# Kernel tuning notes

Measured on AMD Instinct MI355X. Metric: run time of the kernel, lower is better.

## Reference

```python
import jax, jax.numpy as jnp
import numpy as np

N = 50000
E = 800000
IN_C = 128
HID = 8
OUT_C = 32
HEADS = (4, 4, 4)
NEG_SLOPE = 0.2


def gat_conv(x, src, dst, W, att_src, att_dst, bias, heads, out_c, concat):
    # x: [N, F_in]; W: [F_in, heads*out_c]; att_*: [heads, out_c]; bias: [heads*out_c] or [out_c]
    n = x.shape[0]
    h = (x @ W).reshape(n, heads, out_c)                      # [N, H, C]
    a_src = (h * att_src).sum(-1)                             # [N, H]
    a_dst = (h * att_dst).sum(-1)                             # [N, H]
    e = jax.nn.leaky_relu(a_src[src] + a_dst[dst], NEG_SLOPE)  # [E, H]
    # segment softmax over edges grouped by destination node
    m = jax.ops.segment_max(e, dst, num_segments=n)           # [N, H]
    m = jnp.where(jnp.isfinite(m), m, 0.0)
    p = jnp.exp(e - m[dst])                                   # [E, H]
    s = jax.ops.segment_sum(p, dst, num_segments=n)           # [N, H]
    alpha = p / (s[dst] + 1e-16)                              # [E, H]
    msg = h[src] * alpha[:, :, None]                          # [E, H, C]
    out = jax.ops.segment_sum(msg, dst, num_segments=n)       # [N, H, C]
    out = out.reshape(n, heads * out_c) if concat else out.mean(axis=1)
    return out + bias


def setup_inputs() -> dict:
    key = jax.random.key(0)
    ks = jax.random.split(key, 16)
    x = jax.random.normal(ks[0], (N, IN_C), dtype=jnp.float32)
    edge_index = jax.random.randint(ks[1], (2, E), 0, N, dtype=jnp.int64)
    c1 = HID                       # per-head out of conv1 (8)
    c2 = HID * HEADS[0]            # per-head out of conv2 (32)
    c3 = OUT_C                     # per-head out of conv3 (32)
    in2 = HID * HEADS[0]           # 32
    in3 = HID * HEADS[0] * HEADS[1]  # 128
    sc = 0.1
    return {
        "x": x,
        "edge_index": edge_index,
        "W1": jax.random.normal(ks[2], (IN_C, HEADS[0] * c1), dtype=jnp.float32) * sc,
        "as1": jax.random.normal(ks[3], (HEADS[0], c1), dtype=jnp.float32) * sc,
        "ad1": jax.random.normal(ks[4], (HEADS[0], c1), dtype=jnp.float32) * sc,
        "b1": jnp.zeros((HEADS[0] * c1,), dtype=jnp.float32),
        "W2": jax.random.normal(ks[5], (in2, HEADS[1] * c2), dtype=jnp.float32) * sc,
        "as2": jax.random.normal(ks[6], (HEADS[1], c2), dtype=jnp.float32) * sc,
        "ad2": jax.random.normal(ks[7], (HEADS[1], c2), dtype=jnp.float32) * sc,
        "b2": jnp.zeros((HEADS[1] * c2,), dtype=jnp.float32),
        "W3": jax.random.normal(ks[8], (in3, HEADS[2] * c3), dtype=jnp.float32) * sc,
        "as3": jax.random.normal(ks[9], (HEADS[2], c3), dtype=jnp.float32) * sc,
        "ad3": jax.random.normal(ks[10], (HEADS[2], c3), dtype=jnp.float32) * sc,
        "b3": jnp.zeros((c3,), dtype=jnp.float32),
    }


def reference(x, edge_index, W1, as1, ad1, b1, W2, as2, ad2, b2, W3, as3, ad3, b3):
    src, dst = edge_index[0], edge_index[1]
    h = gat_conv(x, src, dst, W1, as1, ad1, b1, HEADS[0], HID, True)
    h = jax.nn.elu(h)
    h = gat_conv(h, src, dst, W2, as2, ad2, b2, HEADS[1], HID * HEADS[0], True)
    h = jax.nn.elu(h)
    out = gat_conv(h, src, dst, W3, as3, ad3, b3, HEADS[2], OUT_C, False)
    return out
```

## Files before the change

kernel.cpp:

```cpp
#include <hip/hip_runtime.h>
#include <hip/hip_fp16.h>

#define NEG_SLOPE 0.2f

static inline int cdiv(long long a, long long b) { return (int)((a + b - 1) / b); }

typedef _Float16 f16x8 __attribute__((ext_vector_type(8)));
typedef float f32x4 __attribute__((ext_vector_type(4)));

__device__ __forceinline__ float4 f4_add(float4 a, float4 b) {
    return make_float4(a.x + b.x, a.y + b.y, a.z + b.z, a.w + b.w);
}
__device__ __forceinline__ float4 f4_leaky(float4 a) {
    return make_float4(a.x > 0.f ? a.x : NEG_SLOPE * a.x,
                       a.y > 0.f ? a.y : NEG_SLOPE * a.y,
                       a.z > 0.f ? a.z : NEG_SLOPE * a.z,
                       a.w > 0.f ? a.w : NEG_SLOPE * a.w);
}
__device__ __forceinline__ float4 f4_exp(float4 e) {
    return make_float4(__expf(e.x), __expf(e.y), __expf(e.z), __expf(e.w));
}
__device__ __forceinline__ float f4_get(float4 v, int i) {
    return i == 0 ? v.x : i == 1 ? v.y : i == 2 ? v.z : v.w;
}

union h4u {
    float2  f2;
    __half2 h2[2];
};

__device__ __forceinline__ void load_sd(const void* ei_raw, int is64, int e, int E_,
                                        int& s, int& d)
{
    if (is64) {
        const long long* p = (const long long*)ei_raw;
        s = (int)p[e];
        d = (int)p[E_ + e];
    } else {
        const int* p = (const int*)ei_raw;
        s = p[e];
        d = p[E_ + e];
    }
}

__global__ __launch_bounds__(256) void prep_kernel(
    const void* __restrict__ ei, int E_, int n, int* __restrict__ flag,
    int* __restrict__ deg,
    const float* __restrict__ W1, __half* __restrict__ Wt1,
    const float* __restrict__ W2, __half* __restrict__ Wt2,
    const float* __restrict__ W3, __half* __restrict__ Wt3)
{
    int idx = blockIdx.x * 256 + threadIdx.x;

    if (blockIdx.x == 0) {
        __shared__ int bad;
        if (threadIdx.x == 0) bad = 0;
        __syncthreads();
        const long long* e64 = (const long long*)ei;
        int cnt = E_ < 512 ? E_ : 512;
        bool ok = true;
        for (int i = threadIdx.x; i < cnt; i += 256) {
            long long v = e64[i];
            if (v < 0 || v >= n) ok = false;
        }
        if (!ok) atomicAdd(&bad, 1);
        __syncthreads();
        if (threadIdx.x == 0) *flag = (bad == 0) ? 1 : 0;
    }

    if (idx < n) deg[idx] = 0;

    if (idx < 128 * 32) {
        int k = idx / 32, c = idx % 32;
        Wt1[c * 128 + k] = __float2half(W1[idx]);
    }
    if (idx < 32 * 128) {
        int k = idx / 128, c = idx % 128;
        Wt2[c * 32 + k] = __float2half(W2[idx]);
    }
    if (idx < 128 * 128) {
        int k = idx / 128, c = idx % 128;
        Wt3[c * 128 + k] = __float2half(W3[idx]);
    }
}

__global__ __launch_bounds__(256) void hist_kernel(const void* __restrict__ ei_raw,
                                                   const int* __restrict__ flag,
                                                   int* __restrict__ deg,
                                                   int* __restrict__ s32,
                                                   int* __restrict__ d32,
                                                   int* __restrict__ rank, int E_)
{
    int base = blockIdx.x * 1024 + threadIdx.x;
    int is64 = *flag;
    int sj[4], dj[4], rj[4];
    bool v[4];
#pragma unroll
    for (int j = 0; j < 4; j++) {
        int e = base + j * 256;
        v[j] = e < E_;
        if (v[j]) load_sd(ei_raw, is64, e, E_, sj[j], dj[j]);
    }
#pragma unroll
    for (int j = 0; j < 4; j++) {
        int e = base + j * 256;
        if (v[j]) { s32[e] = sj[j]; d32[e] = dj[j]; }
    }
#pragma unroll
    for (int j = 0; j < 4; j++) {
        if (v[j]) rj[j] = atomicAdd(deg + dj[j], 1);
    }
#pragma unroll
    for (int j = 0; j < 4; j++) {
        int e = base + j * 256;
        if (v[j]) rank[e] = rj[j];
    }
}

__device__ __forceinline__ int wave_incl_scan(int v)
{
    int lane = threadIdx.x & 63;
#pragma unroll
    for (int off = 1; off < 64; off <<= 1) {
        int t = __shfl_up(v, off);
        if (lane >= off) v += t;
    }
    return v;
}

__global__ __launch_bounds__(1024) void scan_part_kernel(const int* __restrict__ deg,
                                                         int* __restrict__ start,
                                                         int* __restrict__ bsum, int n)
{
    __shared__ int wsum[16];
    int i = blockIdx.x * 1024 + threadIdx.x;
    int wid = threadIdx.x >> 6, lane = threadIdx.x & 63;
    int v = (i < n) ? deg[i] : 0;
    int incl = wave_incl_scan(v);
    if (lane == 63) wsum[wid] = incl;
    __syncthreads();
    if (wid == 0) {
        int w = (lane < 16) ? wsum[lane] : 0;
        w = wave_incl_scan(w);
        if (lane < 16) wsum[lane] = w;
    }
    __syncthreads();
    int excl = incl - v + (wid ? wsum[wid - 1] : 0);
    if (i < n) start[i] = excl;
    if (threadIdx.x == 1023) bsum[blockIdx.x] = wsum[15];
}

__global__ __launch_bounds__(1024) void scan_add_kernel(const int* __restrict__ deg,
                                                        const int* __restrict__ bsum,
                                                        int* __restrict__ start, int n)
{
    __shared__ int off_sh;
    if (threadIdx.x == 0) {
        int s = 0;
        for (int j = 0; j < blockIdx.x; j++) s += bsum[j];
        off_sh = s;
    }
    __syncthreads();
    int i = blockIdx.x * 1024 + threadIdx.x;
    if (i >= n) return;
    int v = start[i] + off_sh;
    start[i] = v;
    if (i == n - 1) start[n] = v + deg[i];
}

__global__ __launch_bounds__(256) void scatter_kernel(const int* __restrict__ s32,
                                                      const int* __restrict__ d32,
                                                      const int* __restrict__ rank,
                                                      const int* __restrict__ start,
                                                      int* __restrict__ sorted_src, int E_)
{
    int base = blockIdx.x * 1024 + threadIdx.x;
    int sj[4], dj[4], rj[4];
    bool v[4];
#pragma unroll
    for (int j = 0; j < 4; j++) {
        int e = base + j * 256;
        v[j] = e < E_;
        sj[j] = v[j] ? s32[e] : 0;
        dj[j] = v[j] ? d32[e] : 0;
        rj[j] = v[j] ? rank[e] : 0;
    }
    int pj[4];
#pragma unroll
    for (int j = 0; j < 4; j++) {
        if (v[j]) pj[j] = start[dj[j]] + rj[j];
    }
#pragma unroll
    for (int j = 0; j < 4; j++) {
        if (v[j]) __builtin_nontemporal_store(sj[j], sorted_src + pj[j]);
    }
}

template <int K, int NOUT, int A16>
__global__ __launch_bounds__(256) void gemm_mfma_kernel(
    const void* __restrict__ xin, const __half* __restrict__ Wt,
    const float* __restrict__ att_s, const float* __restrict__ att_d,
    __half* __restrict__ h, float* __restrict__ a_s, float* __restrict__ a_d, int n)
{
    constexpr int KC = 32;
    constexpr int NT = NOUT / 16;
    constexpr int XP = KC + 8;
    constexpr int HP = NOUT + 8;
    constexpr int C  = NOUT / 4;

    __shared__ _Float16 Xs[64 * XP];
    __shared__ _Float16 Ws[NOUT * XP];
    __shared__ _Float16 Hs[64 * HP];
    __shared__ float As[NOUT], Ad[NOUT];

    const int tid  = threadIdx.x;
    const int nb   = blockIdx.x * 64;
    const int wave = tid >> 6, lane = tid & 63;
    const int m16  = lane & 15, quad = lane >> 4;

    if (tid < NOUT) { As[tid] = att_s[tid]; Ad[tid] = att_d[tid]; }

    f32x4 acc[NT];
#pragma unroll
    for (int t = 0; t < NT; t++) acc[t] = (f32x4){0.f, 0.f, 0.f, 0.f};

    for (int kc = 0; kc < K; kc += KC) {
        {
            int node = tid >> 2, seg = tid & 3;
            int gn = nb + node;
            f16x8 v = {0, 0, 0, 0, 0, 0, 0, 0};
            if (gn < n) {
                if (A16) {
                    v = *(const f16x8*)((const __half*)xin + (size_t)gn * K + kc +
                                        seg * 8);
                } else {
                    const float4* p =
                        (const float4*)((const float*)xin + (size_t)gn * K + kc + seg * 8);
                    float4 a = p[0], b = p[1];
                    v = (f16x8){(_Float16)a.x, (_Float16)a.y, (_Float16)a.z,
                                (_Float16)a.w, (_Float16)b.x, (_Float16)b.y,
                                (_Float16)b.z, (_Float16)b.w};
                }
            }
            *(f16x8*)&Xs[node * XP + seg * 8] = v;
        }
        for (int u = tid; u < NOUT * 4; u += 256) {
            int col = u >> 2, seg = u & 3;
            *(f16x8*)&Ws[col * XP + seg * 8] =
                *(const f16x8*)(Wt + (size_t)col * K + kc + seg * 8);
        }
        __syncthreads();

        f16x8 a = *(const f16x8*)&Xs[(wave * 16 + m16) * XP + quad * 8];
#pragma unroll
        for (int t = 0; t < NT; t++) {
            f16x8 b = *(const f16x8*)&Ws[(t * 16 + m16) * XP + quad * 8];
            acc[t] = __builtin_amdgcn_mfma_f32_16x16x32_f16(a, b, acc[t], 0, 0, 0);
        }
        __syncthreads();
    }

#pragma unroll
    for (int t = 0; t < NT; t++) {
#pragma unroll
        for (int r = 0; r < 4; r++) {
            int row = wave * 16 + quad * 4 + r;
            Hs[row * HP + t * 16 + m16] = (_Float16)acc[t][r];
        }
    }
    __syncthreads();

    for (int u = tid; u < 64 * NOUT / 8; u += 256) {
        int row = u / (NOUT / 8), seg = u % (NOUT / 8);
        int gn = nb + row;
        if (gn < n)
            *(f16x8*)(h + (size_t)gn * NOUT + seg * 8) =
                *(const f16x8*)&Hs[row * HP + seg * 8];
    }

    {
        int node = tid >> 2, head = tid & 3;
        int gn = nb + node;
        const _Float16* hr = &Hs[node * HP + head * C];
        float s1 = 0.f, s2 = 0.f;
#pragma unroll 4
        for (int c = 0; c < C; c++) {
            float v = (float)hr[c];
            s1 += v * As[head * C + c];
            s2 += v * Ad[head * C + c];
        }
        if (gn < n) {
            a_s[gn * 4 + head] = s1;
            a_d[gn * 4 + head] = s2;
        }
    }
}

template <int MODE>
__global__ __launch_bounds__(256) void gat_agg128_kernel(
    const int* __restrict__ start, const int* __restrict__ sorted_src,
    const __half* __restrict__ h, const float* __restrict__ a_s,
    const float* __restrict__ a_d, const float* __restrict__ bias,
    void* __restrict__ out, int n)
{
    constexpr int MAXD = 64;
    __shared__ float  p_sh[8][MAXD * 4];
    __shared__ float4 invs_sh[8];

    int local = threadIdx.x >> 5;
    int q     = threadIdx.x & 31;
    int node  = blockIdx.x * 8 + local;
    bool active = node < n;
    int s0 = 0, s1 = 0;
    if (active) { s0 = start[node]; s1 = start[node + 1]; }
    int deg = s1 - s0;

    const float4* as4 = (const float4*)a_s;
    float4 ad = active ? ((const float4*)a_d)[node] : make_float4(0.f, 0.f, 0.f, 0.f);

    float4 sm = make_float4(0.f, 0.f, 0.f, 0.f);
    for (int i = s0 + q; i < s1; i += 32) {
        int s = sorted_src[i];
        float4 p = f4_exp(f4_leaky(f4_add(as4[s], ad)));
        sm = f4_add(sm, p);
        int j = i - s0;
        if (j < MAXD) ((float4*)&p_sh[local][0])[j] = p;
    }
#pragma unroll
    for (int off = 16; off; off >>= 1) {
        sm.x += __shfl_xor(sm.x, off, 32);
        sm.y += __shfl_xor(sm.y, off, 32);
        sm.z += __shfl_xor(sm.z, off, 32);
        sm.w += __shfl_xor(sm.w, off, 32);
    }
    if (q == 0) {
        invs_sh[local] = make_float4(1.f / (sm.x + 1e-16f), 1.f / (sm.y + 1e-16f),
                                     1.f / (sm.z + 1e-16f), 1.f / (sm.w + 1e-16f));
    }
    __syncthreads();

    int head = q >> 3;
    float invh = f4_get(invs_sh[local], head);
    const float2* __restrict__ h2 = (const float2*)h + q;
    const float* __restrict__ pl = &p_sh[local][0];

    float4 acc = make_float4(0.f, 0.f, 0.f, 0.f);
    if (deg <= MAXD) {
        int i = 0;
        for (; i + 8 <= deg; i += 8) {
            int   sj[8];
            float aj[8];
#pragma unroll
            for (int j = 0; j < 8; j++) sj[j] = sorted_src[s0 + i + j];
#pragma unroll
            for (int j = 0; j < 8; j++) aj[j] = pl[(i + j) * 4 + head] * invh;
            float2 rj[8];
#pragma unroll
            for (int j = 0; j < 8; j++) rj[j] = h2[(size_t)sj[j] * 32];
#pragma unroll
            for (int j = 0; j < 8; j++) {
                h4u u; u.f2 = rj[j];
                float2 lo = __half22float2(u.h2[0]);
                float2 hi = __half22float2(u.h2[1]);
                acc.x += lo.x * aj[j]; acc.y += lo.y * aj[j];
                acc.z += hi.x * aj[j]; acc.w += hi.y * aj[j];
            }
        }
        for (; i < deg; i++) {
            h4u u; u.f2 = h2[(size_t)sorted_src[s0 + i] * 32];
            float a = pl[i * 4 + head] * invh;
            float2 lo = __half22float2(u.h2[0]);
            float2 hi = __half22float2(u.h2[1]);
            acc.x += lo.x * a; acc.y += lo.y * a; acc.z += hi.x * a; acc.w += hi.y * a;
        }
    } else {
        for (int i = s0; i < s1; i++) {
            int s = sorted_src[i];
            float4 p = f4_exp(f4_leaky(f4_add(as4[s], ad)));
            float a = f4_get(p, head) * invh;
            h4u u; u.f2 = h2[(size_t)s * 32];
            float2 lo = __half22float2(u.h2[0]);
            float2 hi = __half22float2(u.h2[1]);
            acc.x += lo.x * a; acc.y += lo.y * a; acc.z += hi.x * a; acc.w += hi.y * a;
        }
    }

    if (MODE == 0) {
        if (active) {
            float4 b4 = ((const float4*)bias)[q];
            float4 v = f4_add(acc, b4);
            v.x = v.x > 0.f ? v.x : (__expf(v.x) - 1.f);
            v.y = v.y > 0.f ? v.y : (__expf(v.y) - 1.f);
            v.z = v.z > 0.f ? v.z : (__expf(v.z) - 1.f);
            v.w = v.w > 0.f ? v.w : (__expf(v.w) - 1.f);
            h4u u;
            u.h2[0] = __floats2half2_rn(v.x, v.y);
            u.h2[1] = __floats2half2_rn(v.z, v.w);
            *(float2*)((__half*)out + (size_t)node * 128 + q * 4) = u.f2;
        }
    } else {
        __shared__ float4 sh4[8][33];
        sh4[local][q] = acc;
        __syncthreads();
        if (q < 8 && active) {
            float4 a = sh4[local][q];
            float4 b = sh4[local][q + 8];
            float4 c = sh4[local][q + 16];
            float4 d = sh4[local][q + 24];
            float4 b4 = ((const float4*)bias)[q];
            float4 r = make_float4(0.25f * (a.x + b.x + c.x + d.x) + b4.x,
                                   0.25f * (a.y + b.y + c.y + d.y) + b4.y,
                                   0.25f * (a.z + b.z + c.z + d.z) + b4.z,
                                   0.25f * (a.w + b.w + c.w + d.w) + b4.w);
            *(float4*)((float*)out + (size_t)node * 32 + q * 4) = r;
        }
    }
}

__global__ __launch_bounds__(256) void gat_agg32_kernel(
    const int* __restrict__ start, const int* __restrict__ sorted_src,
    const __half* __restrict__ h, const float* __restrict__ a_s,
    const float* __restrict__ a_d, const float* __restrict__ bias,
    __half* __restrict__ out, int n)
{
    constexpr int MAXD = 32;
    __shared__ float  p_sh[32][MAXD * 4];
    __shared__ float4 invs_sh[32];

    int local = threadIdx.x >> 3;
    int q     = threadIdx.x & 7;
    int node  = blockIdx.x * 32 + local;
    bool active = node < n;
    int s0 = 0, s1 = 0;
    if (active) { s0 = start[node]; s1 = start[node + 1]; }
    int deg = s1 - s0;

    const float4* as4 = (const float4*)a_s;
    float4 ad = active ? ((const float4*)a_d)[node] : make_float4(0.f, 0.f, 0.f, 0.f);

    float4 sm = make_float4(0.f, 0.f, 0.f, 0.f);
    for (int i = s0 + q; i < s1; i += 8) {
        int s = sorted_src[i];
        float4 p = f4_exp(f4_leaky(f4_add(as4[s], ad)));
        sm = f4_add(sm, p);
        int j = i - s0;
        if (j < MAXD) ((float4*)&p_sh[local][0])[j] = p;
    }
#pragma unroll
    for (int off = 4; off; off >>= 1) {
        sm.x += __shfl_xor(sm.x, off, 8);
        sm.y += __shfl_xor(sm.y, off, 8);
        sm.z += __shfl_xor(sm.z, off, 8);
        sm.w += __shfl_xor(sm.w, off, 8);
    }
    if (q == 0) {
        invs_sh[local] = make_float4(1.f / (sm.x + 1e-16f), 1.f / (sm.y + 1e-16f),
                                     1.f / (sm.z + 1e-16f), 1.f / (sm.w + 1e-16f));
    }
    __syncthreads();

    int head = q >> 1;
    float invh = f4_get(invs_sh[local], head);
    const float2* __restrict__ h2 = (const float2*)h + q;
    const float* __restrict__ pl = &p_sh[local][0];

    float4 acc = make_float4(0.f, 0.f, 0.f, 0.f);
    if (deg <= MAXD) {
        int i = 0;
        for (; i + 8 <= deg; i += 8) {
            int   sj[8];
            float aj[8];
#pragma unroll
            for (int j = 0; j < 8; j++) sj[j] = sorted_src[s0 + i + j];
#pragma unroll
            for (int j = 0; j < 8; j++) aj[j] = pl[(i + j) * 4 + head] * invh;
            float2 rj[8];
#pragma unroll
            for (int j = 0; j < 8; j++) rj[j] = h2[(size_t)sj[j] * 8];
#pragma unroll
            for (int j = 0; j < 8; j++) {
                h4u u; u.f2 = rj[j];
                float2 lo = __half22float2(u.h2[0]);
                float2 hi = __half22float2(u.h2[1]);
                acc.x += lo.x * aj[j]; acc.y += lo.y * aj[j];
                acc.z += hi.x * aj[j]; acc.w += hi.y * aj[j];
            }
        }
        for (; i < deg; i++) {
            h4u u; u.f2 = h2[(size_t)sorted_src[s0 + i] * 8];
            float a = pl[i * 4 + head] * invh;
            float2 lo = __half22float2(u.h2[0]);
            float2 hi = __half22float2(u.h2[1]);
            acc.x += lo.x * a; acc.y += lo.y * a; acc.z += hi.x * a; acc.w += hi.y * a;
        }
    } else {
        for (int i = s0; i < s1; i++) {
            int s = sorted_src[i];
            float4 p = f4_exp(f4_leaky(f4_add(as4[s], ad)));
            float a = f4_get(p, head) * invh;
            h4u u; u.f2 = h2[(size_t)s * 8];
            float2 lo = __half22float2(u.h2[0]);
            float2 hi = __half22float2(u.h2[1]);
            acc.x += lo.x * a; acc.y += lo.y * a; acc.z += hi.x * a; acc.w += hi.y * a;
        }
    }

    if (active) {
        float4 b4 = ((const float4*)bias)[q];
        float4 v = f4_add(acc, b4);
        v.x = v.x > 0.f ? v.x : (__expf(v.x) - 1.f);
        v.y = v.y > 0.f ? v.y : (__expf(v.y) - 1.f);
        v.z = v.z > 0.f ? v.z : (__expf(v.z) - 1.f);
        v.w = v.w > 0.f ? v.w : (__expf(v.w) - 1.f);
        h4u u;
        u.h2[0] = __floats2half2_rn(v.x, v.y);
        u.h2[1] = __floats2half2_rn(v.z, v.w);
        *(float2*)(out + (size_t)node * 32 + q * 4) = u.f2;
    }
}


extern "C" void kernel_launch(void* const* d_in, const int* in_sizes, int n_in,
                              void* d_out, int out_size, void* d_ws, size_t ws_size,
                              hipStream_t stream)
{
    const float* x   = (const float*)d_in[0];
    const void*  ei  = d_in[1];
    const float* W1  = (const float*)d_in[2];
    const float* as1 = (const float*)d_in[3];
    const float* ad1 = (const float*)d_in[4];
    const float* b1  = (const float*)d_in[5];
    const float* W2  = (const float*)d_in[6];
    const float* as2 = (const float*)d_in[7];
    const float* ad2 = (const float*)d_in[8];
    const float* b2  = (const float*)d_in[9];
    const float* W3  = (const float*)d_in[10];
    const float* as3 = (const float*)d_in[11];
    const float* ad3 = (const float*)d_in[12];
    const float* b3  = (const float*)d_in[13];
    float* out = (float*)d_out;

    const int N_ = in_sizes[0] / 128;
    const int E_ = in_sizes[1] / 2;

    char* ws = (char*)d_ws;
    size_t off = 0;
    auto alloc = [&](size_t nbytes) -> void* {
        void* p = ws + off;
        off += (nbytes + 255) & ~(size_t)255;
        return p;
    };
    __half* h         = (__half*)alloc((size_t)N_ * 128 * 2);
    __half* x2h       = (__half*)alloc((size_t)N_ * 32 * 2);
    __half* x3h       = (__half*)alloc((size_t)N_ * 128 * 2);
    __half* Wt1       = (__half*)alloc(128 * 32 * 2);
    __half* Wt2       = (__half*)alloc(32 * 128 * 2);
    __half* Wt3       = (__half*)alloc(128 * 128 * 2);
    float* asrc       = (float*)alloc((size_t)N_ * 4 * 4);
    float* adst       = (float*)alloc((size_t)N_ * 4 * 4);
    int*   deg        = (int*)alloc((size_t)N_ * 4);
    int*   start      = (int*)alloc((size_t)(N_ + 1) * 4);
    int*   sorted_src = (int*)alloc((size_t)E_ * 4);
    int*   s32        = (int*)alloc((size_t)E_ * 4);
    int*   d32        = (int*)alloc((size_t)E_ * 4);
    int*   rank       = (int*)alloc((size_t)E_ * 4);
    int*   bsum       = (int*)alloc(4096);
    int*   flag       = (int*)alloc(256);

    const int gN8  = cdiv(N_, 8);
    const int gN32 = cdiv(N_, 32);
    const int gN64 = cdiv(N_, 64);
    const int nSB  = cdiv(N_, 1024);
    int prepWork = N_ > 128 * 128 ? N_ : 128 * 128;

    prep_kernel<<<cdiv(prepWork, 256), 256, 0, stream>>>(ei, E_, N_, flag, deg,
                                                         W1, Wt1, W2, Wt2, W3, Wt3);
    hist_kernel<<<cdiv(E_, 1024), 256, 0, stream>>>(ei, flag, deg, s32, d32, rank, E_);
    scan_part_kernel<<<nSB, 1024, 0, stream>>>(deg, start, bsum, N_);
    scan_add_kernel<<<nSB, 1024, 0, stream>>>(deg, bsum, start, N_);
    scatter_kernel<<<cdiv(E_, 1024), 256, 0, stream>>>(s32, d32, rank, start,
                                                       sorted_src, E_);

    gemm_mfma_kernel<128, 32, 0><<<gN64, 256, 0, stream>>>(x, Wt1, as1, ad1, h,
                                                           asrc, adst, N_);
    gat_agg32_kernel<<<gN32, 256, 0, stream>>>(start, sorted_src, h, asrc, adst, b1,
                                               x2h, N_);

    gemm_mfma_kernel<32, 128, 1><<<gN64, 256, 0, stream>>>(x2h, Wt2, as2, ad2, h,
                                                           asrc, adst, N_);
    gat_agg128_kernel<0><<<gN8, 256, 0, stream>>>(start, sorted_src, h, asrc, adst, b2,
                                                  x3h, N_);

    gemm_mfma_kernel<128, 128, 1><<<gN64, 256, 0, stream>>>(x3h, Wt3, as3, ad3, h,
                                                            asrc, adst, N_);
    gat_agg128_kernel<1><<<gN8, 256, 0, stream>>>(start, sorted_src, h, asrc, adst, b3,
                                                  out, N_);
}
```

Before: 313.0 us.

## Use 16-bit edge indices and single-pass online softmax in GAT aggregation

```diff
diff --git a/kernel.cpp b/kernel.cpp
--- a/kernel.cpp
+++ b/kernel.cpp
@@ -7,22 +7,6 @@
 
 typedef _Float16 f16x8 __attribute__((ext_vector_type(8)));
 typedef float f32x4 __attribute__((ext_vector_type(4)));
-
-__device__ __forceinline__ float4 f4_add(float4 a, float4 b) {
-    return make_float4(a.x + b.x, a.y + b.y, a.z + b.z, a.w + b.w);
-}
-__device__ __forceinline__ float4 f4_leaky(float4 a) {
-    return make_float4(a.x > 0.f ? a.x : NEG_SLOPE * a.x,
-                       a.y > 0.f ? a.y : NEG_SLOPE * a.y,
-                       a.z > 0.f ? a.z : NEG_SLOPE * a.z,
-                       a.w > 0.f ? a.w : NEG_SLOPE * a.w);
-}
-__device__ __forceinline__ float4 f4_exp(float4 e) {
-    return make_float4(__expf(e.x), __expf(e.y), __expf(e.z), __expf(e.w));
-}
-__device__ __forceinline__ float f4_get(float4 v, int i) {
-    return i == 0 ? v.x : i == 1 ? v.y : i == 2 ? v.z : v.w;
-}
 
 union h4u {
     float2  f2;
@@ -87,9 +71,10 @@
 __global__ __launch_bounds__(256) void hist_kernel(const void* __restrict__ ei_raw,
                                                    const int* __restrict__ flag,
                                                    int* __restrict__ deg,
-                                                   int* __restrict__ s32,
-                                                   int* __restrict__ d32,
-                                                   int* __restrict__ rank, int E_)
+                                                   unsigned short* __restrict__ s16,
+                                                   unsigned short* __restrict__ d16,
+                                                   unsigned short* __restrict__ r16,
+                                                   int E_)
 {
     int base = blockIdx.x * 1024 + threadIdx.x;
     int is64 = *flag;
@@ -104,7 +89,10 @@
 #pragma unroll
     for (int j = 0; j < 4; j++) {
         int e = base + j * 256;
-        if (v[j]) { s32[e] = sj[j]; d32[e] = dj[j]; }
+        if (v[j]) {
+            s16[e] = (unsigned short)sj[j];
+            d16[e] = (unsigned short)dj[j];
+        }
     }
 #pragma unroll
     for (int j = 0; j < 4; j++) {
@@ -113,7 +101,7 @@
 #pragma unroll
     for (int j = 0; j < 4; j++) {
         int e = base + j * 256;
-        if (v[j]) rank[e] = rj[j];
+        if (v[j]) r16[e] = (unsigned short)rj[j];
     }
 }
 
@@ -168,11 +156,10 @@
     if (i == n - 1) start[n] = v + deg[i];
 }
 
-__global__ __launch_bounds__(256) void scatter_kernel(const int* __restrict__ s32,
-                                                      const int* __restrict__ d32,
-                                                      const int* __restrict__ rank,
-                                                      const int* __restrict__ start,
-                                                      int* __restrict__ sorted_src, int E_)
+__global__ __launch_bounds__(256) void scatter_kernel(
+    const unsigned short* __restrict__ s16, const unsigned short* __restrict__ d16,
+    const unsigned short* __restrict__ r16, const int* __restrict__ start,
+    unsigned short* __restrict__ sorted_src, int E_)
 {
     int base = blockIdx.x * 1024 + threadIdx.x;
     int sj[4], dj[4], rj[4];
@@ -181,9 +168,9 @@
     for (int j = 0; j < 4; j++) {
         int e = base + j * 256;
         v[j] = e < E_;
-        sj[j] = v[j] ? s32[e] : 0;
-        dj[j] = v[j] ? d32[e] : 0;
-        rj[j] = v[j] ? rank[e] : 0;
+        sj[j] = v[j] ? (int)s16[e] : 0;
+        dj[j] = v[j] ? (int)d16[e] : 0;
+        rj[j] = v[j] ? (int)r16[e] : 0;
     }
     int pj[4];
 #pragma unroll
@@ -192,7 +179,8 @@
     }
 #pragma unroll
     for (int j = 0; j < 4; j++) {
-        if (v[j]) __builtin_nontemporal_store(sj[j], sorted_src + pj[j]);
+        if (v[j])
+            __builtin_nontemporal_store((unsigned short)sj[j], sorted_src + pj[j]);
     }
 }
 
@@ -298,97 +286,68 @@
 
 template <int MODE>
 __global__ __launch_bounds__(256) void gat_agg128_kernel(
-    const int* __restrict__ start, const int* __restrict__ sorted_src,
+    const int* __restrict__ start, const unsigned short* __restrict__ ss,
     const __half* __restrict__ h, const float* __restrict__ a_s,
     const float* __restrict__ a_d, const float* __restrict__ bias,
     void* __restrict__ out, int n)
 {
-    constexpr int MAXD = 64;
-    __shared__ float  p_sh[8][MAXD * 4];
-    __shared__ float4 invs_sh[8];
-
     int local = threadIdx.x >> 5;
     int q     = threadIdx.x & 31;
     int node  = blockIdx.x * 8 + local;
     bool active = node < n;
     int s0 = 0, s1 = 0;
     if (active) { s0 = start[node]; s1 = start[node + 1]; }
-    int deg = s1 - s0;
-
-    const float4* as4 = (const float4*)a_s;
-    float4 ad = active ? ((const float4*)a_d)[node] : make_float4(0.f, 0.f, 0.f, 0.f);
-
-    float4 sm = make_float4(0.f, 0.f, 0.f, 0.f);
-    for (int i = s0 + q; i < s1; i += 32) {
-        int s = sorted_src[i];
-        float4 p = f4_exp(f4_leaky(f4_add(as4[s], ad)));
-        sm = f4_add(sm, p);
-        int j = i - s0;
-        if (j < MAXD) ((float4*)&p_sh[local][0])[j] = p;
-    }
-#pragma unroll
-    for (int off = 16; off; off >>= 1) {
-        sm.x += __shfl_xor(sm.x, off, 32);
-        sm.y += __shfl_xor(sm.y, off, 32);
-        sm.z += __shfl_xor(sm.z, off, 32);
-        sm.w += __shfl_xor(sm.w, off, 32);
-    }
-    if (q == 0) {
-        invs_sh[local] = make_float4(1.f / (sm.x + 1e-16f), 1.f / (sm.y + 1e-16f),
-                                     1.f / (sm.z + 1e-16f), 1.f / (sm.w + 1e-16f));
-    }
-    __syncthreads();
-
     int head = q >> 3;
-    float invh = f4_get(invs_sh[local], head);
+    float adh = active ? a_d[node * 4 + head] : 0.f;
     const float2* __restrict__ h2 = (const float2*)h + q;
-    const float* __restrict__ pl = &p_sh[local][0];
 
     float4 acc = make_float4(0.f, 0.f, 0.f, 0.f);
-    if (deg <= MAXD) {
-        int i = 0;
-        for (; i + 8 <= deg; i += 8) {
-            int   sj[8];
-            float aj[8];
-#pragma unroll
-            for (int j = 0; j < 8; j++) sj[j] = sorted_src[s0 + i + j];
-#pragma unroll
-            for (int j = 0; j < 8; j++) aj[j] = pl[(i + j) * 4 + head] * invh;
-            float2 rj[8];
-#pragma unroll
-            for (int j = 0; j < 8; j++) rj[j] = h2[(size_t)sj[j] * 32];
-#pragma unroll
-            for (int j = 0; j < 8; j++) {
-                h4u u; u.f2 = rj[j];
-                float2 lo = __half22float2(u.h2[0]);
-                float2 hi = __half22float2(u.h2[1]);
-                acc.x += lo.x * aj[j]; acc.y += lo.y * aj[j];
-                acc.z += hi.x * aj[j]; acc.w += hi.y * aj[j];
-            }
-        }
-        for (; i < deg; i++) {
-            h4u u; u.f2 = h2[(size_t)sorted_src[s0 + i] * 32];
-            float a = pl[i * 4 + head] * invh;
+    float sm = 0.f;
+    int i = s0;
+    for (; i + 8 <= s1; i += 8) {
+        int    sj[8];
+        float  ej[8];
+        float2 rj[8];
+#pragma unroll
+        for (int j = 0; j < 8; j++) sj[j] = (int)ss[i + j];
+#pragma unroll
+        for (int j = 0; j < 8; j++) ej[j] = a_s[sj[j] * 4 + head];
+#pragma unroll
+        for (int j = 0; j < 8; j++) rj[j] = h2[(size_t)sj[j] * 32];
+#pragma unroll
+        for (int j = 0; j < 8; j++) {
+            float e = ej[j] + adh;
+            e = e > 0.f ? e : NEG_SLOPE * e;
+            float p = __expf(e);
+            sm += p;
+            h4u u; u.f2 = rj[j];
             float2 lo = __half22float2(u.h2[0]);
             float2 hi = __half22float2(u.h2[1]);
-            acc.x += lo.x * a; acc.y += lo.y * a; acc.z += hi.x * a; acc.w += hi.y * a;
-        }
-    } else {
-        for (int i = s0; i < s1; i++) {
-            int s = sorted_src[i];
-            float4 p = f4_exp(f4_leaky(f4_add(as4[s], ad)));
-            float a = f4_get(p, head) * invh;
-            h4u u; u.f2 = h2[(size_t)s * 32];
-            float2 lo = __half22float2(u.h2[0]);
-            float2 hi = __half22float2(u.h2[1]);
-            acc.x += lo.x * a; acc.y += lo.y * a; acc.z += hi.x * a; acc.w += hi.y * a;
-        }
-    }
+            acc.x += lo.x * p; acc.y += lo.y * p;
+            acc.z += hi.x * p; acc.w += hi.y * p;
+        }
+    }
+    for (; i < s1; i++) {
+        int s = (int)ss[i];
+        float e = a_s[s * 4 + head] + adh;
+        e = e > 0.f ? e : NEG_SLOPE * e;
+        float p = __expf(e);
+        sm += p;
+        h4u u; u.f2 = h2[(size_t)s * 32];
+        float2 lo = __half22float2(u.h2[0]);
+        float2 hi = __half22float2(u.h2[1]);
+        acc.x += lo.x * p; acc.y += lo.y * p;
+        acc.z += hi.x * p; acc.w += hi.y * p;
+    }
+
+    float inv = 1.f / (sm + 1e-16f);
+    acc.x *= inv; acc.y *= inv; acc.z *= inv; acc.w *= inv;
 
     if (MODE == 0) {
         if (active) {
             float4 b4 = ((const float4*)bias)[q];
-            float4 v = f4_add(acc, b4);
+            float4 v = make_float4(acc.x + b4.x, acc.y + b4.y, acc.z + b4.z,
+                                   acc.w + b4.w);
             v.x = v.x > 0.f ? v.x : (__expf(v.x) - 1.f);
             v.y = v.y > 0.f ? v.y : (__expf(v.y) - 1.f);
             v.z = v.z > 0.f ? v.z : (__expf(v.z) - 1.f);
@@ -418,96 +377,65 @@
 }
 
 __global__ __launch_bounds__(256) void gat_agg32_kernel(
-    const int* __restrict__ start, const int* __restrict__ sorted_src,
+    const int* __restrict__ start, const unsigned short* __restrict__ ss,
     const __half* __restrict__ h, const float* __restrict__ a_s,
     const float* __restrict__ a_d, const float* __restrict__ bias,
     __half* __restrict__ out, int n)
 {
-    constexpr int MAXD = 32;
-    __shared__ float  p_sh[32][MAXD * 4];
-    __shared__ float4 invs_sh[32];
-
     int local = threadIdx.x >> 3;
     int q     = threadIdx.x & 7;
     int node  = blockIdx.x * 32 + local;
     bool active = node < n;
     int s0 = 0, s1 = 0;
     if (active) { s0 = start[node]; s1 = start[node + 1]; }
-    int deg = s1 - s0;
-
-    const float4* as4 = (const float4*)a_s;
-    float4 ad = active ? ((const float4*)a_d)[node] : make_float4(0.f, 0.f, 0.f, 0.f);
-
-    float4 sm = make_float4(0.f, 0.f, 0.f, 0.f);
-    for (int i = s0 + q; i < s1; i += 8) {
-        int s = sorted_src[i];
-        float4 p = f4_exp(f4_leaky(f4_add(as4[s], ad)));
-        sm = f4_add(sm, p);
-        int j = i - s0;
-        if (j < MAXD) ((float4*)&p_sh[local][0])[j] = p;
-    }
-#pragma unroll
-    for (int off = 4; off; off >>= 1) {
-        sm.x += __shfl_xor(sm.x, off, 8);
-        sm.y += __shfl_xor(sm.y, off, 8);
-        sm.z += __shfl_xor(sm.z, off, 8);
-        sm.w += __shfl_xor(sm.w, off, 8);
-    }
-    if (q == 0) {
-        invs_sh[local] = make_float4(1.f / (sm.x + 1e-16f), 1.f / (sm.y + 1e-16f),
-                                     1.f / (sm.z + 1e-16f), 1.f / (sm.w + 1e-16f));
-    }
-    __syncthreads();
-
     int head = q >> 1;
-    float invh = f4_get(invs_sh[local], head);
+    float adh = active ? a_d[node * 4 + head] : 0.f;
     const float2* __restrict__ h2 = (const float2*)h + q;
-    const float* __restrict__ pl = &p_sh[local][0];
 
     float4 acc = make_float4(0.f, 0.f, 0.f, 0.f);
-    if (deg <= MAXD) {
-        int i = 0;
-        for (; i + 8 <= deg; i += 8) {
-            int   sj[8];
-            float aj[8];
-#pragma unroll
-            for (int j = 0; j < 8; j++) sj[j] = sorted_src[s0 + i + j];
-#pragma unroll
-            for (int j = 0; j < 8; j++) aj[j] = pl[(i + j) * 4 + head] * invh;
-            float2 rj[8];
-#pragma unroll
-            for (int j = 0; j < 8; j++) rj[j] = h2[(size_t)sj[j] * 8];
-#pragma unroll
-            for (int j = 0; j < 8; j++) {
-                h4u u; u.f2 = rj[j];
-                float2 lo = __half22float2(u.h2[0]);
-                float2 hi = __half22float2(u.h2[1]);
-                acc.x += lo.x * aj[j]; acc.y += lo.y * aj[j];
-                acc.z += hi.x * aj[j]; acc.w += hi.y * aj[j];
-            }
-        }
-        for (; i < deg; i++) {
-            h4u u; u.f2 = h2[(size_t)sorted_src[s0 + i] * 8];
-            float a = pl[i * 4 + head] * invh;
+    float sm = 0.f;
+    int i = s0;
+    for (; i + 8 <= s1; i += 8) {
+        int    sj[8];
+        float  ej[8];
+        float2 rj[8];
+#pragma unroll
+        for (int j = 0; j < 8; j++) sj[j] = (int)ss[i + j];
+#pragma unroll
+        for (int j = 0; j < 8; j++) ej[j] = a_s[sj[j] * 4 + head];
+#pragma unroll
+        for (int j = 0; j < 8; j++) rj[j] = h2[(size_t)sj[j] * 8];
+#pragma unroll
+        for (int j = 0; j < 8; j++) {
+            float e = ej[j] + adh;
+            e = e > 0.f ? e : NEG_SLOPE * e;
+            float p = __expf(e);
+            sm += p;
+            h4u u; u.f2 = rj[j];
             float2 lo = __half22float2(u.h2[0]);
             float2 hi = __half22float2(u.h2[1]);
-            acc.x += lo.x * a; acc.y += lo.y * a; acc.z += hi.x * a; acc.w += hi.y * a;
-        }
-    } else {
-        for (int i = s0; i < s1; i++) {
-            int s = sorted_src[i];
-            float4 p = f4_exp(f4_leaky(f4_add(as4[s], ad)));
-            float a = f4_get(p, head) * invh;
-            h4u u; u.f2 = h2[(size_t)s * 8];
-            float2 lo = __half22float2(u.h2[0]);
-            float2 hi = __half22float2(u.h2[1]);
-            acc.x += lo.x * a; acc.y += lo.y * a; acc.z += hi.x * a; acc.w += hi.y * a;
-        }
+            acc.x += lo.x * p; acc.y += lo.y * p;
+            acc.z += hi.x * p; acc.w += hi.y * p;
+        }
+    }
+    for (; i < s1; i++) {
+        int s = (int)ss[i];
+        float e = a_s[s * 4 + head] + adh;
+        e = e > 0.f ? e : NEG_SLOPE * e;
+        float p = __expf(e);
+        sm += p;
+        h4u u; u.f2 = h2[(size_t)s * 8];
+        float2 lo = __half22float2(u.h2[0]);
+        float2 hi = __half22float2(u.h2[1]);
+        acc.x += lo.x * p; acc.y += lo.y * p;
+        acc.z += hi.x * p; acc.w += hi.y * p;
     }
 
     if (active) {
+        float inv = 1.f / (sm + 1e-16f);
         float4 b4 = ((const float4*)bias)[q];
-        float4 v = f4_add(acc, b4);
+        float4 v = make_float4(acc.x * inv + b4.x, acc.y * inv + b4.y,
+                               acc.z * inv + b4.z, acc.w * inv + b4.w);
         v.x = v.x > 0.f ? v.x : (__expf(v.x) - 1.f);
         v.y = v.y > 0.f ? v.y : (__expf(v.y) - 1.f);
         v.z = v.z > 0.f ? v.z : (__expf(v.z) - 1.f);
@@ -550,22 +478,22 @@
         off += (nbytes + 255) & ~(size_t)255;
         return p;
     };
-    __half* h         = (__half*)alloc((size_t)N_ * 128 * 2);
-    __half* x2h       = (__half*)alloc((size_t)N_ * 32 * 2);
-    __half* x3h       = (__half*)alloc((size_t)N_ * 128 * 2);
-    __half* Wt1       = (__half*)alloc(128 * 32 * 2);
-    __half* Wt2       = (__half*)alloc(32 * 128 * 2);
-    __half* Wt3       = (__half*)alloc(128 * 128 * 2);
-    float* asrc       = (float*)alloc((size_t)N_ * 4 * 4);
-    float* adst       = (float*)alloc((size_t)N_ * 4 * 4);
-    int*   deg        = (int*)alloc((size_t)N_ * 4);
-    int*   start      = (int*)alloc((size_t)(N_ + 1) * 4);
-    int*   sorted_src = (int*)alloc((size_t)E_ * 4);
-    int*   s32        = (int*)alloc((size_t)E_ * 4);
-    int*   d32        = (int*)alloc((size_t)E_ * 4);
-    int*   rank       = (int*)alloc((size_t)E_ * 4);
-    int*   bsum       = (int*)alloc(4096);
-    int*   flag       = (int*)alloc(256);
+    __half* h          = (__half*)alloc((size_t)N_ * 128 * 2);
+    __half* x2h        = (__half*)alloc((size_t)N_ * 32 * 2);
+    __half* x3h        = (__half*)alloc((size_t)N_ * 128 * 2);
+    __half* Wt1        = (__half*)alloc(128 * 32 * 2);
+    __half* Wt2        = (__half*)alloc(32 * 128 * 2);
+    __half* Wt3        = (__half*)alloc(128 * 128 * 2);
+    float* asrc        = (float*)alloc((size_t)N_ * 4 * 4);
+    float* adst        = (float*)alloc((size_t)N_ * 4 * 4);
+    int*   deg         = (int*)alloc((size_t)N_ * 4);
+    int*   start       = (int*)alloc((size_t)(N_ + 1) * 4);
+    unsigned short* sorted_src = (unsigned short*)alloc((size_t)E_ * 2);
+    unsigned short* s16        = (unsigned short*)alloc((size_t)E_ * 2);
+    unsigned short* d16        = (unsigned short*)alloc((size_t)E_ * 2);
+    unsigned short* r16        = (unsigned short*)alloc((size_t)E_ * 2);
+    int*   bsum        = (int*)alloc(4096);
+    int*   flag        = (int*)alloc(256);
 
     const int gN8  = cdiv(N_, 8);
     const int gN32 = cdiv(N_, 32);
@@ -575,10 +503,10 @@
 
     prep_kernel<<<cdiv(prepWork, 256), 256, 0, stream>>>(ei, E_, N_, flag, deg,
                                                          W1, Wt1, W2, Wt2, W3, Wt3);
-    hist_kernel<<<cdiv(E_, 1024), 256, 0, stream>>>(ei, flag, deg, s32, d32, rank, E_);
+    hist_kernel<<<cdiv(E_, 1024), 256, 0, stream>>>(ei, flag, deg, s16, d16, r16, E_);
     scan_part_kernel<<<nSB, 1024, 0, stream>>>(deg, start, bsum, N_);
     scan_add_kernel<<<nSB, 1024, 0, stream>>>(deg, bsum, start, N_);
-    scatter_kernel<<<cdiv(E_, 1024), 256, 0, stream>>>(s32, d32, rank, start,
+    scatter_kernel<<<cdiv(E_, 1024), 256, 0, stream>>>(s16, d16, r16, start,
                                                        sorted_src, E_);
 
     gemm_mfma_kernel<128, 32, 0><<<gN64, 256, 0, stream>>>(x, Wt1, as1, ad1, h,
```

Measured after the change: 285.9 us. 1.09x faster.
